# Kernel optimization log

Hardware: AMD Instinct MI355X
Metric: run time of the kernel (lower is better)

The kernel has to match this reference:

```python
import jax, jax.numpy as jnp
import numpy as np

D_MODEL = 1024
NUM_HEADS = 16
D_K = D_MODEL // NUM_HEADS
ROPE_THETA = 10000.0


def apply_rope(x, positions):
    # x: [b, h, s, d_k]; positions: [b, s] int
    half = x.shape[-1] // 2
    inv_freq = 1.0 / (ROPE_THETA ** (jnp.arange(half, dtype=jnp.float32) * 2.0 / x.shape[-1]))
    ang = positions.astype(jnp.float32)[..., None] * inv_freq  # [b, s, half]
    cos = jnp.cos(ang)[:, None, :, :]  # [b, 1, s, half]
    sin = jnp.sin(ang)[:, None, :, :]
    x1 = x[..., 0::2]
    x2 = x[..., 1::2]
    r1 = x1 * cos - x2 * sin
    r2 = x1 * sin + x2 * cos
    # interleave back
    out = jnp.stack([r1, r2], axis=-1).reshape(x.shape)
    return out


def setup_inputs() -> dict:
    key = jax.random.key(0)
    k1, k2, k3 = jax.random.split(key, 3)
    b, s = 4, 2048
    x = jax.random.normal(k1, (b, s, D_MODEL), dtype=jnp.float32)
    token_positions = jnp.broadcast_to(jnp.arange(s, dtype=jnp.int32), (b, s))
    w_qkv = jax.random.normal(k2, (3 * D_MODEL, D_MODEL), dtype=jnp.float32) * (D_MODEL ** -0.5)
    w_o = jax.random.normal(k3, (D_MODEL, D_MODEL), dtype=jnp.float32) * (D_MODEL ** -0.5)
    return {"x": x, "token_positions": token_positions, "w_qkv": w_qkv, "w_o": w_o}


def reference(x, token_positions, w_qkv, w_o):
    b, s, _ = x.shape
    qkv = jnp.einsum('bsd,ed->bse', x, w_qkv)  # [b, s, 3*H*Dk]
    qkv = qkv.reshape(b, s, 3, NUM_HEADS, D_K).transpose(2, 0, 3, 1, 4)  # [3, b, H, s, Dk]
    q, k, v = qkv[0], qkv[1], qkv[2]
    q = apply_rope(q, token_positions)
    k = apply_rope(k, token_positions)
    scale = 1.0 / jnp.sqrt(jnp.float32(D_K))
    scores = jnp.einsum('bhqd,bhkd->bhqk', q, k) * scale
    causal = jnp.tril(jnp.ones((s, s), dtype=bool))
    scores = jnp.where(causal, scores, -jnp.inf)
    attn = jax.nn.softmax(scores, axis=-1)
    out = jnp.einsum('bhqk,bhkd->bhqd', attn, v)  # [b, H, s, Dk]
    out = out.transpose(0, 2, 1, 3).reshape(b, s, D_MODEL)
    return jnp.einsum('bse,de->bsd', out, w_o)
```

## Files before the change

### kernel.cpp

```cpp
#include <hip/hip_runtime.h>
#include <math.h>

typedef __bf16 bf16x8 __attribute__((ext_vector_type(8)));
typedef __bf16 bf16x4 __attribute__((ext_vector_type(4)));
typedef float  floatx4 __attribute__((ext_vector_type(4)));
typedef unsigned short ushortx8 __attribute__((ext_vector_type(8)));

#define D_MODEL 1024
#define NQKV 3072
#define SEQ 2048
#define BATCH 4
#define NH 16
#define DKD 64
#define MTOT (BATCH*SEQ)

#define SCALE_L2E 0.18033688011112042f
#define FIXED_M 16.0f

__device__ __forceinline__ unsigned short f2bf(float f) {
  unsigned int u = __float_as_uint(f);
  u += 0x7FFFu + ((u >> 16) & 1u);
  return (unsigned short)(u >> 16);
}

__device__ __forceinline__ float dpp_swap1(float v) {
  int i = __builtin_amdgcn_mov_dpp(__float_as_int(v), 0xB1, 0xF, 0xF, true);
  return __int_as_float(i);
}

__device__ __forceinline__ void gld16(unsigned short* lds, const unsigned short* g) {
  __builtin_amdgcn_global_load_lds(
      (const __attribute__((address_space(1))) unsigned int*)g,
      (__attribute__((address_space(3))) unsigned int*)lds, 16, 0, 0);
}

__global__ void cvt_kernel(const float4* __restrict__ in, ushort4* __restrict__ out, int n4) {
  int i = blockIdx.x * blockDim.x + threadIdx.x;
  if (i < n4) {
    float4 v = in[i];
    ushort4 o;
    o.x = f2bf(v.x); o.y = f2bf(v.y); o.z = f2bf(v.z); o.w = f2bf(v.w);
    out[i] = o;
  }
}

template<int EPI>
__global__ __launch_bounds__(256) void gemm_bt(
    const unsigned short* __restrict__ A,
    const unsigned short* __restrict__ B,
    float* __restrict__ C, int K, int N,
    const int* __restrict__ pos,
    unsigned short* __restrict__ qb,
    unsigned short* __restrict__ kb,
    unsigned short* __restrict__ vb)
{
  __shared__ unsigned short As[128*32];
  __shared__ unsigned short Bs[128*32];
  const int tid = threadIdx.x;
  const int wave = tid >> 6, lane = tid & 63;
  const int l16 = lane & 15, quad = lane >> 4;
  const int wr = wave >> 1, wc = wave & 1;
  const int bm = blockIdx.x * 128, bn = blockIdx.y * 128;

  floatx4 acc[4][4] = {};
  const int srow = tid >> 2;
  const int scol = (tid & 3) * 8;
  const unsigned short* Ag = A + (size_t)(bm + srow) * K + scol;
  const unsigned short* Bg = B + (size_t)(bn + srow) * K + scol;
  unsigned short* Al = &As[tid * 8];
  unsigned short* Bl = &Bs[tid * 8];
  const size_t pstep = (size_t)64 * K;

  for (int k0 = 0; k0 < K; k0 += 32) {
    __syncthreads();
    gld16(Al,        Ag + k0);
    gld16(Al + 2048, Ag + k0 + pstep);
    gld16(Bl,        Bg + k0);
    gld16(Bl + 2048, Bg + k0 + pstep);
    __syncthreads();
    bf16x8 a[4], b[4];
#pragma unroll
    for (int i = 0; i < 4; ++i) a[i] = *(const bf16x8*)&As[(wr*64 + i*16 + l16)*32 + quad*8];
#pragma unroll
    for (int t = 0; t < 4; ++t) b[t] = *(const bf16x8*)&Bs[(wc*64 + t*16 + l16)*32 + quad*8];
#pragma unroll
    for (int i = 0; i < 4; ++i)
#pragma unroll
      for (int t = 0; t < 4; ++t)
        acc[i][t] = __builtin_amdgcn_mfma_f32_16x16x32_bf16(a[i], b[t], acc[i][t], 0, 0, 0);
  }

  if (EPI == 0) {
#pragma unroll
    for (int i = 0; i < 4; ++i)
#pragma unroll
      for (int r = 0; r < 4; ++r) {
        int row = bm + wr*64 + i*16 + quad*4 + r;
#pragma unroll
        for (int t = 0; t < 4; ++t) {
          int col = bn + wc*64 + t*16 + l16;
          C[(size_t)row * N + col] = acc[i][t][r];
        }
      }
  } else {
    const int which = bn >> 10;
    int h_t[4], dk_t[4];
#pragma unroll
    for (int t = 0; t < 4; ++t) {
      int col = bn + wc*64 + t*16 + l16;
      h_t[t]  = (col >> 6) & 15;
      dk_t[t] = col & 63;
    }
    if (which == 2) {
#pragma unroll
      for (int i = 0; i < 4; ++i) {
        int row0 = bm + wr*64 + i*16 + quad*4;
        int b = row0 >> 11, s0 = row0 & 2047;
#pragma unroll
        for (int t = 0; t < 4; ++t) {
          union { bf16x4 v; uint2 u; } pk;
#pragma unroll
          for (int r = 0; r < 4; ++r) pk.v[r] = (__bf16)acc[i][t][r];
          *(uint2*)&vb[((size_t)((b << 4) + h_t[t]) * DKD + dk_t[t]) * SEQ + s0] = pk.u;
        }
      }
    } else {
      float inv_t[4];
#pragma unroll
      for (int t = 0; t < 4; ++t)
        inv_t[t] = exp2f((float)(dk_t[t] >> 1) * (-13.287712379549449f / 32.0f));
      unsigned short* dstp = (which == 0) ? qb : kb;
#pragma unroll
      for (int i = 0; i < 4; ++i)
#pragma unroll
        for (int r = 0; r < 4; ++r) {
          int row = bm + wr*64 + i*16 + quad*4 + r;
          int b = row >> 11, s = row & 2047;
          float p = (float)pos[row];
#pragma unroll
          for (int t = 0; t < 4; ++t) {
            float val = acc[i][t][r];
            size_t dst = ((size_t)((b << 4) + h_t[t]) * SEQ + s) * DKD + dk_t[t];
            float partner = dpp_swap1(val);
            float ang = p * inv_t[t];
            float sn, cs;
            __sincosf(ang, &sn, &cs);
            float rr = (lane & 1) ? (partner * sn + val * cs)
                                  : (val * cs - partner * sn);
            if (which == 0) rr *= SCALE_L2E;
            dstp[dst] = f2bf(rr);
          }
        }
    }
  }
}

__global__ __launch_bounds__(256) void attn_kernel(
    const unsigned short* __restrict__ qb,
    const unsigned short* __restrict__ kb,
    const unsigned short* __restrict__ vb,
    unsigned short* __restrict__ ob)
{
  __shared__ unsigned short Ks[128*64];
  __shared__ unsigned short Vt[64*128];
  __shared__ unsigned short Ps[128*72];
  const int tid = threadIdx.x;
  const int wave = tid >> 6, lane = tid & 63;
  const int l16 = lane & 15, quad = lane >> 4;
  const int l8 = l16 & 7;
  const int id = blockIdx.x;
  const int bh = id & 63;
  const int qtb = 15 - (id >> 6);
  const int qbase = qtb * 128;
  const int rounds = qtb + 1;
  const size_t base = (size_t)bh * SEQ * DKD;
  const int bb = bh >> 4, hh0 = bh & 15;

  bf16x8 vones;
#pragma unroll
  for (int j = 0; j < 8; ++j) vones[j] = (__bf16)1.0f;

  const int kx0 = (quad ^ l8) * 8;
  const int kx1 = ((4 + quad) ^ l8) * 8;

  int ksrc[4], vsrc[4];
#pragma unroll
  for (int u = 0; u < 4; ++u) {
    int task = tid + u*256;
    int kr_ = task >> 3, kc_ = (task & 7) ^ (kr_ & 7);
    ksrc[u] = kr_*DKD + kc_*8;
    int vr_ = task >> 4, vc_ = (task & 15) ^ (vr_ & 7);
    vsrc[u] = vr_*SEQ + vc_*8;
  }

  bf16x8 qf[2][2];
#pragma unroll
  for (int f = 0; f < 2; ++f)
#pragma unroll
    for (int hh = 0; hh < 2; ++hh)
      qf[f][hh] = *(const bf16x8*)&qb[base + (size_t)(qbase + f*64 + wave*16 + l16)*DKD + hh*32 + quad*8];

  floatx4 o[2][4] = {};
  floatx4 ls[2] = {};

  for (int kt = 0; kt < rounds; ++kt) {
    const unsigned short* kg = kb + base + (size_t)kt * 128 * DKD;
    const unsigned short* vg = vb + base + kt * 128;
    __syncthreads();
#pragma unroll
    for (int u = 0; u < 4; ++u) {
      gld16(&Ks[(tid + u*256)*8], kg + ksrc[u]);
      gld16(&Vt[(tid + u*256)*8], vg + vsrc[u]);
    }
    __syncthreads();
    const bool diag = (kt == rounds - 1);
#pragma unroll
    for (int ch = 0; ch < 2; ++ch) {
      floatx4 sc[2][4];
#pragma unroll
      for (int f = 0; f < 2; ++f)
#pragma unroll
        for (int tl = 0; tl < 4; ++tl)
          sc[f][tl] = (floatx4){-FIXED_M, -FIXED_M, -FIXED_M, -FIXED_M};
#pragma unroll
      for (int tl = 0; tl < 4; ++tl) {
        int t = ch*4 + tl;
        const int krow = (t*16 + l16)*64;
        bf16x8 ka0 = *(const bf16x8*)&Ks[krow + kx0];
        bf16x8 ka1 = *(const bf16x8*)&Ks[krow + kx1];
        sc[0][tl] = __builtin_amdgcn_mfma_f32_16x16x32_bf16(ka0, qf[0][0], sc[0][tl], 0, 0, 0);
        sc[0][tl] = __builtin_amdgcn_mfma_f32_16x16x32_bf16(ka1, qf[0][1], sc[0][tl], 0, 0, 0);
        sc[1][tl] = __builtin_amdgcn_mfma_f32_16x16x32_bf16(ka0, qf[1][0], sc[1][tl], 0, 0, 0);
        sc[1][tl] = __builtin_amdgcn_mfma_f32_16x16x32_bf16(ka1, qf[1][1], sc[1][tl], 0, 0, 0);
      }
#pragma unroll
      for (int f = 0; f < 2; ++f) {
        const int qrl = f*64 + wave*16 + l16;
#pragma unroll
        for (int tl = 0; tl < 4; ++tl) {
          int t = ch*4 + tl;
          union { bf16x4 v; uint2 u; } pk;
#pragma unroll
          for (int r = 0; r < 4; ++r) {
            float s = sc[f][tl][r];
            if (diag && (t*16 + quad*4 + r > qrl)) s = -INFINITY;
            pk.v[r] = (__bf16)__builtin_amdgcn_exp2f(s);
          }
          *(uint2*)&Ps[(f*64 + wave*16 + l16)*72 + tl*16 + quad*4] = pk.u;
        }
      }
      bf16x8 pf[2][2];
#pragma unroll
      for (int f = 0; f < 2; ++f)
#pragma unroll
        for (int cl = 0; cl < 2; ++cl)
          pf[f][cl] = *(const bf16x8*)&Ps[(f*64 + wave*16 + l16)*72 + cl*32 + quad*8];
#pragma unroll
      for (int cl = 0; cl < 2; ++cl) {
        int c = ch*2 + cl;
        __builtin_amdgcn_s_setprio(1);
#pragma unroll
        for (int t = 0; t < 4; ++t) {
          int d = t*16 + l16;
          bf16x8 vf = *(const bf16x8*)&Vt[d*128 + (((c*4 + quad) ^ l8) * 8)];
          o[0][t] = __builtin_amdgcn_mfma_f32_16x16x32_bf16(vf, pf[0][cl], o[0][t], 0, 0, 0);
          o[1][t] = __builtin_amdgcn_mfma_f32_16x16x32_bf16(vf, pf[1][cl], o[1][t], 0, 0, 0);
        }
        ls[0] = __builtin_amdgcn_mfma_f32_16x16x32_bf16(vones, pf[0][cl], ls[0], 0, 0, 0);
        ls[1] = __builtin_amdgcn_mfma_f32_16x16x32_bf16(vones, pf[1][cl], ls[1], 0, 0, 0);
        __builtin_amdgcn_s_setprio(0);
      }
    }
  }

#pragma unroll
  for (int f = 0; f < 2; ++f) {
    int qrow = qbase + f*64 + wave*16 + l16;
    float invl = 1.0f / ls[f][0];
    size_t rb = ((size_t)bb * SEQ + qrow) * D_MODEL + hh0*DKD;
#pragma unroll
    for (int t = 0; t < 4; ++t) {
      union { bf16x4 v; uint2 u; } pk;
#pragma unroll
      for (int r = 0; r < 4; ++r) pk.v[r] = (__bf16)(o[f][t][r] * invl);
      *(uint2*)&ob[rb + t*16 + quad*4] = pk.u;
    }
  }
}

extern "C" void kernel_launch(void* const* d_in, const int* in_sizes, int n_in,
                              void* d_out, int out_size, void* d_ws, size_t ws_size,
                              hipStream_t stream) {
  const float* x    = (const float*)d_in[0];
  const int*   pos  = (const int*)d_in[1];
  const float* wqkv = (const float*)d_in[2];
  const float* wo   = (const float*)d_in[3];

  char* ws = (char*)d_ws;
  unsigned short* xb    = (unsigned short*)(ws);
  unsigned short* wqkvb = (unsigned short*)(ws + 16777216);
  unsigned short* wob   = (unsigned short*)(ws + 23068672);
  unsigned short* qb    = (unsigned short*)(ws + 25165824);
  unsigned short* kb    = (unsigned short*)(ws + 41943040);
  unsigned short* vb    = (unsigned short*)(ws + 58720256);
  unsigned short* ab    = (unsigned short*)(ws + 75497472);

  int nx  = MTOT * D_MODEL;
  int nwq = NQKV * D_MODEL;
  int nwo = D_MODEL * D_MODEL;
  cvt_kernel<<<(nx/4 + 255)/256, 256, 0, stream>>>((const float4*)x, (ushort4*)xb, nx/4);
  cvt_kernel<<<(nwq/4 + 255)/256, 256, 0, stream>>>((const float4*)wqkv, (ushort4*)wqkvb, nwq/4);
  cvt_kernel<<<(nwo/4 + 255)/256, 256, 0, stream>>>((const float4*)wo, (ushort4*)wob, nwo/4);

  gemm_bt<1><<<dim3(MTOT/128, NQKV/128), 256, 0, stream>>>(
      xb, wqkvb, (float*)nullptr, D_MODEL, NQKV, pos, qb, kb, vb);

  attn_kernel<<<dim3(1024), 256, 0, stream>>>(qb, kb, vb, ab);

  gemm_bt<0><<<dim3(MTOT/128, D_MODEL/128), 256, 0, stream>>>(
      ab, wob, (float*)d_out, D_MODEL, D_MODEL, nullptr, nullptr, nullptr, nullptr);
}
```

Before: 251.5 us.

## Double GEMM K-tile to 64 with XOR-swizzled LDS and pack RoPE stores

The bf16 GEMM now stages a 64-wide K slice per iteration instead of 32. Each thread issues four 16-byte loads per operand, and the LDS layout is XOR-swizzled by row so the MFMA fragment reads avoid bank conflicts. This halves the number of barrier pairs per K loop, at the cost of doubling LDS per block. In the RoPE epilogue, each even lane computes both rotated outputs of a pair and writes them as one 32-bit store, so odd lanes no longer issue scattered 16-bit stores.

```diff
diff --git a/kernel.cpp b/kernel.cpp
--- a/kernel.cpp
+++ b/kernel.cpp
@@ -54,8 +54,8 @@
     unsigned short* __restrict__ kb,
     unsigned short* __restrict__ vb)
 {
-  __shared__ unsigned short As[128*32];
-  __shared__ unsigned short Bs[128*32];
+  __shared__ unsigned short As[128*64];
+  __shared__ unsigned short Bs[128*64];
   const int tid = threadIdx.x;
   const int wave = tid >> 6, lane = tid & 63;
   const int l16 = lane & 15, quad = lane >> 4;
@@ -63,31 +63,43 @@
   const int bm = blockIdx.x * 128, bn = blockIdx.y * 128;
 
   floatx4 acc[4][4] = {};
-  const int srow = tid >> 2;
-  const int scol = (tid & 3) * 8;
-  const unsigned short* Ag = A + (size_t)(bm + srow) * K + scol;
-  const unsigned short* Bg = B + (size_t)(bn + srow) * K + scol;
+
+  int offA[4], offB[4];
+#pragma unroll
+  for (int u = 0; u < 4; ++u) {
+    int task = tid + u*256;
+    int row = task >> 3;
+    int c   = (task & 7) ^ (row & 7);
+    offA[u] = (bm + row) * K + c*8;
+    offB[u] = (bn + row) * K + c*8;
+  }
   unsigned short* Al = &As[tid * 8];
   unsigned short* Bl = &Bs[tid * 8];
-  const size_t pstep = (size_t)64 * K;
-
-  for (int k0 = 0; k0 < K; k0 += 32) {
+  const int x0 = ((quad)     ^ (l16 & 7)) * 8;
+  const int x1 = ((4 + quad) ^ (l16 & 7)) * 8;
+
+  for (int k0 = 0; k0 < K; k0 += 64) {
     __syncthreads();
-    gld16(Al,        Ag + k0);
-    gld16(Al + 2048, Ag + k0 + pstep);
-    gld16(Bl,        Bg + k0);
-    gld16(Bl + 2048, Bg + k0 + pstep);
+#pragma unroll
+    for (int u = 0; u < 4; ++u) {
+      gld16(Al + u*2048, A + offA[u] + k0);
+      gld16(Bl + u*2048, B + offB[u] + k0);
+    }
     __syncthreads();
-    bf16x8 a[4], b[4];
-#pragma unroll
-    for (int i = 0; i < 4; ++i) a[i] = *(const bf16x8*)&As[(wr*64 + i*16 + l16)*32 + quad*8];
-#pragma unroll
-    for (int t = 0; t < 4; ++t) b[t] = *(const bf16x8*)&Bs[(wc*64 + t*16 + l16)*32 + quad*8];
-#pragma unroll
-    for (int i = 0; i < 4; ++i)
-#pragma unroll
-      for (int t = 0; t < 4; ++t)
-        acc[i][t] = __builtin_amdgcn_mfma_f32_16x16x32_bf16(a[i], b[t], acc[i][t], 0, 0, 0);
+#pragma unroll
+    for (int kk = 0; kk < 2; ++kk) {
+      const int xo = kk ? x1 : x0;
+      bf16x8 a[4], b[4];
+#pragma unroll
+      for (int i = 0; i < 4; ++i) a[i] = *(const bf16x8*)&As[(wr*64 + i*16 + l16)*64 + xo];
+#pragma unroll
+      for (int t = 0; t < 4; ++t) b[t] = *(const bf16x8*)&Bs[(wc*64 + t*16 + l16)*64 + xo];
+#pragma unroll
+      for (int i = 0; i < 4; ++i)
+#pragma unroll
+        for (int t = 0; t < 4; ++t)
+          acc[i][t] = __builtin_amdgcn_mfma_f32_16x16x32_bf16(a[i], b[t], acc[i][t], 0, 0, 0);
+    }
   }
 
   if (EPI == 0) {
@@ -130,6 +142,7 @@
       for (int t = 0; t < 4; ++t)
         inv_t[t] = exp2f((float)(dk_t[t] >> 1) * (-13.287712379549449f / 32.0f));
       unsigned short* dstp = (which == 0) ? qb : kb;
+      const bool evenlane = (lane & 1) == 0;
 #pragma unroll
       for (int i = 0; i < 4; ++i)
 #pragma unroll
@@ -140,15 +153,19 @@
 #pragma unroll
           for (int t = 0; t < 4; ++t) {
             float val = acc[i][t][r];
-            size_t dst = ((size_t)((b << 4) + h_t[t]) * SEQ + s) * DKD + dk_t[t];
             float partner = dpp_swap1(val);
             float ang = p * inv_t[t];
             float sn, cs;
             __sincosf(ang, &sn, &cs);
-            float rr = (lane & 1) ? (partner * sn + val * cs)
-                                  : (val * cs - partner * sn);
-            if (which == 0) rr *= SCALE_L2E;
-            dstp[dst] = f2bf(rr);
+            float r1 = val * cs - partner * sn;
+            float r2 = val * sn + partner * cs;
+            if (which == 0) { r1 *= SCALE_L2E; r2 *= SCALE_L2E; }
+            union { __bf16 h[2]; unsigned int u; } pk2;
+            pk2.h[0] = (__bf16)r1; pk2.h[1] = (__bf16)r2;
+            if (evenlane) {
+              size_t dst = ((size_t)((b << 4) + h_t[t]) * SEQ + s) * DKD + dk_t[t];
+              *(unsigned int*)&dstp[dst] = pk2.u;
+            }
           }
         }
     }
```

Measured after the change: 250.8 us. Within noise of the previous version (-0.3%).
